# Kernel optimization log

Hardware: AMD Instinct MI355X
Metric: run time of the kernel (lower is better)

The kernel has to match this reference:

```python
import jax, jax.numpy as jnp
import numpy as np

B, T, D_IN, D_HID, D_OUT, N_CAT = 128, 64, 1024, 1024, 1536, 32


def setup_inputs() -> dict:
    key = jax.random.key(0)
    kx, kw1, kw2, kc = jax.random.split(key, 4)
    x = jax.random.normal(kx, (B, T, D_IN), dtype=jnp.float32)
    W1 = 0.02 * jax.random.normal(kw1, (N_CAT, D_IN, D_HID), dtype=jnp.float32)
    b1 = jnp.zeros((N_CAT, D_HID), dtype=jnp.float32)
    W2 = 0.02 * jax.random.normal(kw2, (N_CAT, D_HID, D_OUT), dtype=jnp.float32)
    b2 = jnp.zeros((N_CAT, D_OUT), dtype=jnp.float32)
    cat_ids = jax.random.randint(kc, (B,), 0, N_CAT)
    return {"x": x, "W1": W1, "b1": b1, "W2": W2, "b2": b2, "cat_ids": cat_ids}


def reference(x, W1, b1, W2, b2, cat_ids):
    # CategorySpecificLinear: gather per-sample expert weights, then batched matmul.
    # Layer 1: (B,T,D_in) @ (B,D_in,D_hid) + (B,1,D_hid)
    h = jnp.einsum('btd,bdh->bth', x, W1[cat_ids]) + b1[cat_ids][:, None, :]
    h = jax.nn.relu(h)
    # Layer 2: (B,T,D_hid) @ (B,D_hid,D_out) + (B,1,D_out)
    out = jnp.einsum('bth,bho->bto', h, W2[cat_ids]) + b2[cat_ids][:, None, :]
    return out
```

## Files before the change

kernel.cpp:

```cpp
#include <hip/hip_runtime.h>
#include <stdint.h>

#define NB    128
#define TT    64
#define KTOT  1024
#define DHID  1024
#define DOUT  1536
#define NCAT  32

#define BK    64
#define TN    128
#define PADR  72
#define NGMAX 64

typedef unsigned short u16;
typedef __attribute__((ext_vector_type(8))) short bf16x8;
typedef __attribute__((ext_vector_type(4))) float f32x4;
typedef __attribute__((ext_vector_type(4))) unsigned int uint4v;
typedef __attribute__((ext_vector_type(4))) float float4v;

__device__ __forceinline__ float bf2f(u16 u) {
    unsigned int x = ((unsigned int)u) << 16;
    return __builtin_bit_cast(float, x);
}
__device__ __forceinline__ unsigned int f2bf_u32(float f) {
    unsigned int x = __builtin_bit_cast(unsigned int, f);
    return (x + 0x7FFFu + ((x >> 16) & 1u)) >> 16;
}
__device__ __forceinline__ u16 f2bf(float f) { return (u16)f2bf_u32(f); }

__device__ int g_is_f32;

__global__ void detect_dtype(const unsigned int* __restrict__ xw) {
    const int lane = threadIdx.x;
    const unsigned int w = xw[lane * 64];
    const unsigned int e = (w >> 7) & 0xFF;
    const unsigned long long m = __ballot(e >= 120 && e <= 132);
    if (lane == 0) g_is_f32 = (__popcll(m) < 32) ? 1 : 0;
}

__device__ __forceinline__ void gload16(const void* g, void* l) {
    __builtin_amdgcn_global_load_lds(
        (const __attribute__((address_space(1))) void*)g,
        (__attribute__((address_space(3))) void*)l, 16, 0, 0);
}

__global__ void prep_x(const void* __restrict__ x, u16* __restrict__ xb) {
    const bool f32 = (g_is_f32 != 0);
    const size_t base = ((size_t)blockIdx.x * 256 + threadIdx.x) * 8;
    if (f32) {
        const float* s = (const float*)x + base;
        float4v f0 = *(const float4v*)s;
        float4v f1 = *(const float4v*)(s + 4);
        uint4v v;
        v.x = f2bf_u32(f0.x) | (f2bf_u32(f0.y) << 16);
        v.y = f2bf_u32(f0.z) | (f2bf_u32(f0.w) << 16);
        v.z = f2bf_u32(f1.x) | (f2bf_u32(f1.y) << 16);
        v.w = f2bf_u32(f1.z) | (f2bf_u32(f1.w) << 16);
        *(uint4v*)&xb[base] = v;
    } else {
        *(uint4v*)&xb[base] = *(const uint4v*)((const u16*)x + base);
    }
}

__global__ void build_groups(const int* __restrict__ cid,
                             int* __restrict__ gcat, int* __restrict__ gbat) {
    __shared__ int cl[NB];
    __shared__ int cnt[NCAT], start[NCAT], gbase[NCAT];
    __shared__ int sorted[NB];
    const int t = threadIdx.x;
    cl[t] = cid[t];
    if (t < NGMAX) gcat[t] = -1;
    gbat[t] = -1; gbat[NB + t] = -1;
    __syncthreads();
    if (t < NCAT) {
        int c = 0;
        for (int i = 0; i < NB; ++i) c += (cl[i] == t) ? 1 : 0;
        cnt[t] = c;
    }
    __syncthreads();
    if (t == 0) {
        int s = 0, g = 0;
        for (int c = 0; c < NCAT; ++c) {
            start[c] = s; s += cnt[c];
            gbase[c] = g; g += (cnt[c] + 3) >> 2;
        }
    }
    __syncthreads();
    {
        const int myc = cl[t];
        int r = 0;
        for (int i = 0; i < t; ++i) r += (cl[i] == myc) ? 1 : 0;
        sorted[start[myc] + r] = t;
    }
    __syncthreads();
    if (t < NCAT) {
        const int n = cnt[t], ng = (n + 3) >> 2;
        for (int j = 0; j < ng; ++j) {
            const int g = gbase[t] + j;
            gcat[g] = t;
            for (int k = 0; k < 4; ++k) {
                const int idx = j * 4 + k;
                gbat[g * 4 + k] = (idx < n) ? sorted[start[t] + idx] : -1;
            }
        }
    }
}

template<int NW, bool RELU, bool OUT_DYN>
__global__ __launch_bounds__(512, 4)
void gemm_grp(const u16* __restrict__ A,
              const void* __restrict__ Win,
              const void* __restrict__ BiasIn,
              void* __restrict__ Cout,
              const int* __restrict__ gcat,
              const int* __restrict__ gbat)
{
    constexpr int NT   = NW / TN;
    constexpr int NTIL = KTOT / 32;
    __shared__ __align__(16) u16 As[2][4 * TT * 32];
    __shared__ __align__(16) u16 Bs[2][TN * 32];

    const int nwg = NGMAX * NT;
    int bid = blockIdx.x;
    bid = (bid & 7) * (nwg >> 3) + (bid >> 3);
    const int g   = bid / NT;
    const int nt  = bid % NT;
    const int cat = gcat[g];
    if (cat < 0) return;

    const bool f32 = (g_is_f32 != 0);
    const int t    = threadIdx.x;
    const int wave = t >> 6;
    const int lane = t & 63;
    const int l16  = lane & 15;
    const int q    = lane >> 4;
    const int wm   = wave & 1;
    const int wn   = wave >> 1;

    const int bslot[4] = { gbat[g*4+0], gbat[g*4+1], gbat[g*4+2], gbat[g*4+3] };

    const int tt   = t & 255;
    const int arow = tt >> 2;
    const int asc  = (((tt & 3) ^ ((tt >> 2) & 3) ^ ((tt >> 4) & 3)) << 3);
    const int ah   = wave >> 2;
    const int sA0  = ah, sA1 = 2 + ah;
    const u16* aG0 = (bslot[sA0] >= 0)
        ? (A + (size_t)bslot[sA0] * (TT * KTOT) + (size_t)arow * KTOT + asc) : (const u16*)0;
    const u16* aG1 = (bslot[sA1] >= 0)
        ? (A + (size_t)bslot[sA1] * (TT * KTOT) + (size_t)arow * KTOT + asc) : (const u16*)0;

    const int bn  = t & 127;
    const int kc  = t >> 7;
    const int wch = ((kc ^ (bn & 3) ^ ((bn >> 2) & 3)) << 4);
    const size_t wOff = (size_t)cat * ((size_t)KTOT * NW) + (size_t)(kc * 8) * NW
                        + (size_t)nt * TN + bn;
    const float* w32 = (const float*)Win + wOff;
    const u16*   w16 = (const u16*)Win + wOff;

    const int CH = ((q ^ (l16 & 3) ^ ((l16 >> 2) & 3)) << 4);

    f32x4 acc[4][2][2];
#pragma unroll
    for (int bt = 0; bt < 4; ++bt)
#pragma unroll
        for (int im = 0; im < 2; ++im)
#pragma unroll
            for (int in = 0; in < 2; ++in)
                acc[bt][im][in] = (f32x4){0.f, 0.f, 0.f, 0.f};

    unsigned int wr[8];

    auto W_ISSUE = [&](int kk) {
        if (f32) {
            const float* ws = w32 + (size_t)kk * NW;
#pragma unroll
            for (int j = 0; j < 8; ++j)
                wr[j] = __builtin_bit_cast(unsigned int, ws[(size_t)j * NW]);
        } else {
            const u16* ws = w16 + (size_t)kk * NW;
#pragma unroll
            for (int j = 0; j < 8; ++j) wr[j] = ws[(size_t)j * NW];
        }
    };
    auto W_PACK = [&](int pb) {
        unsigned int p[4];
#pragma unroll
        for (int i = 0; i < 4; ++i) {
            unsigned int lo, hi;
            if (f32) {
                lo = f2bf_u32(__builtin_bit_cast(float, wr[2*i]));
                hi = f2bf_u32(__builtin_bit_cast(float, wr[2*i+1]));
            } else { lo = wr[2*i]; hi = wr[2*i+1]; }
            p[i] = lo | (hi << 16);
        }
        uint4v v; v.x = p[0]; v.y = p[1]; v.z = p[2]; v.w = p[3];
        *(uint4v*)((char*)&Bs[pb][0] + bn * 64 + wch) = v;
    };
    auto A_ISSUE = [&](int pb, int kk) {
        char* ab = (char*)&As[pb][0] + wave * 1024;
        if (aG0) gload16(aG0 + kk, ab);
        if (aG1) gload16(aG1 + kk, ab + 8192);
    };
    auto COMPUTE = [&](int pb) {
        const char* bsb = (const char*)&Bs[pb][0];
        const int nrow = wn * 32 + l16;
        bf16x8 bb0 = *(const bf16x8*)(bsb + nrow * 64 + CH);
        bf16x8 bb1 = *(const bf16x8*)(bsb + (nrow + 16) * 64 + CH);
        const char* asb = (const char*)&As[pb][0] + (wm * 32 + l16) * 64 + CH;
#pragma unroll
        for (int bt = 0; bt < 4; ++bt) {
            bf16x8 a0 = *(const bf16x8*)(asb + bt * 4096);
            bf16x8 a1 = *(const bf16x8*)(asb + bt * 4096 + 1024);
            acc[bt][0][0] = __builtin_amdgcn_mfma_f32_16x16x32_bf16(a0, bb0, acc[bt][0][0], 0, 0, 0);
            acc[bt][0][1] = __builtin_amdgcn_mfma_f32_16x16x32_bf16(a0, bb1, acc[bt][0][1], 0, 0, 0);
            acc[bt][1][0] = __builtin_amdgcn_mfma_f32_16x16x32_bf16(a1, bb0, acc[bt][1][0], 0, 0, 0);
            acc[bt][1][1] = __builtin_amdgcn_mfma_f32_16x16x32_bf16(a1, bb1, acc[bt][1][1], 0, 0, 0);
        }
    };

    W_ISSUE(0);
    A_ISSUE(0, 0);
    W_PACK(0);
    __syncthreads();

#pragma unroll 2
    for (int tl = 0; tl < NTIL; ++tl) {
        const int cur = tl & 1;
        if (tl + 1 < NTIL) {
            W_ISSUE((tl + 1) * 32);
            A_ISSUE(cur ^ 1, (tl + 1) * 32);
        }
        COMPUTE(cur);
        if (tl + 1 < NTIL) W_PACK(cur ^ 1);
        __syncthreads();
    }

    const float* bias32 = (const float*)BiasIn + (size_t)cat * NW + (size_t)nt * TN;
    const u16*   bias16 = (const u16*)BiasIn + (size_t)cat * NW + (size_t)nt * TN;
#pragma unroll
    for (int in = 0; in < 2; ++in) {
        const int ncol = wn * 32 + in * 16 + l16;
        const float bv = f32 ? bias32[ncol] : bf2f(bias16[ncol]);
#pragma unroll
        for (int bt = 0; bt < 4; ++bt) {
            const int b = bslot[bt];
            if (b < 0) continue;
            const size_t cOff = (size_t)b * (TT * NW) + (size_t)nt * TN + ncol;
#pragma unroll
            for (int im = 0; im < 2; ++im) {
#pragma unroll
                for (int r = 0; r < 4; ++r) {
                    const int m = wm * 32 + im * 16 + q * 4 + r;
                    float v = acc[bt][im][in][r] + bv;
                    if (RELU) v = fmaxf(v, 0.f);
                    if (OUT_DYN && f32) ((float*)Cout)[cOff + (size_t)m * NW] = v;
                    else                ((u16*)Cout)[cOff + (size_t)m * NW] = f2bf(v);
                }
            }
        }
    }
}

template<int NW, bool RELU, bool A_DYN, bool OUT_DYN>
__global__ __launch_bounds__(256, 4)
void gemm_cat(const void* __restrict__ Ain,
              const void* __restrict__ Win,
              const void* __restrict__ BiasIn,
              void* __restrict__ Cout,
              const int* __restrict__ cat_ids)
{
    constexpr int NT = NW / TN;
    __shared__ u16 As[TT * PADR];
    __shared__ u16 Bs[TN * PADR];

    const bool f32  = (g_is_f32 != 0);
    const bool aF32 = A_DYN && f32;
    const bool oF32 = OUT_DYN && f32;

    const int b   = blockIdx.x / NT;
    const int nt  = blockIdx.x % NT;
    const int cat = cat_ids[b];

    const int tid  = threadIdx.x;
    const int lane = tid & 63;
    const int l16  = lane & 15;
    const int q    = lane >> 4;
    const int wave = tid >> 6;
    const int wm   = wave & 1;
    const int wn   = wave >> 1;

    const size_t aOff = (size_t)b * (TT * KTOT);
    const u16*   Ab16 = (const u16*)Ain + aOff;
    const float* Ab32 = (const float*)Ain + aOff;
    const size_t wOff = (size_t)cat * ((size_t)KTOT * NW) + (size_t)nt * TN;
    const u16*   Wb16 = (const u16*)Win + wOff;
    const float* Wb32 = (const float*)Win + wOff;

    const int ar = tid >> 2;
    const int ac = (tid & 3) * 16;
    const int bn  = tid & 127;
    const int bk0 = tid >> 7;

    f32x4 acc[2][4];
#pragma unroll
    for (int im = 0; im < 2; ++im)
#pragma unroll
        for (int in = 0; in < 4; ++in)
            acc[im][in] = (f32x4){0.f, 0.f, 0.f, 0.f};

    for (int kk = 0; kk < KTOT; kk += BK) {
        if (!aF32) {
            const u16* src = Ab16 + ar * KTOT + kk + ac;
            uint4v v0 = *(const uint4v*)(src);
            uint4v v1 = *(const uint4v*)(src + 8);
            *(uint4v*)&As[ar * PADR + ac]     = v0;
            *(uint4v*)&As[ar * PADR + ac + 8] = v1;
        } else {
            const float* src = Ab32 + ar * KTOT + kk + ac;
            float4v f0 = *(const float4v*)(src);
            float4v f1 = *(const float4v*)(src + 4);
            float4v f2 = *(const float4v*)(src + 8);
            float4v f3 = *(const float4v*)(src + 12);
            uint4v v0, v1;
            v0.x = f2bf_u32(f0.x) | (f2bf_u32(f0.y) << 16);
            v0.y = f2bf_u32(f0.z) | (f2bf_u32(f0.w) << 16);
            v0.z = f2bf_u32(f1.x) | (f2bf_u32(f1.y) << 16);
            v0.w = f2bf_u32(f1.z) | (f2bf_u32(f1.w) << 16);
            v1.x = f2bf_u32(f2.x) | (f2bf_u32(f2.y) << 16);
            v1.y = f2bf_u32(f2.z) | (f2bf_u32(f2.w) << 16);
            v1.z = f2bf_u32(f3.x) | (f2bf_u32(f3.y) << 16);
            v1.w = f2bf_u32(f3.z) | (f2bf_u32(f3.w) << 16);
            *(uint4v*)&As[ar * PADR + ac]     = v0;
            *(uint4v*)&As[ar * PADR + ac + 8] = v1;
        }
#pragma unroll
        for (int i = 0; i < 4; ++i) {
            const int kc = bk0 + i * 2;
            unsigned int s[8];
            if (!f32) {
                const u16* src = Wb16 + (size_t)(kk + kc * 8) * NW + bn;
#pragma unroll
                for (int j = 0; j < 8; ++j) s[j] = src[(size_t)j * NW];
            } else {
                const float* src = Wb32 + (size_t)(kk + kc * 8) * NW + bn;
#pragma unroll
                for (int j = 0; j < 8; ++j) s[j] = f2bf_u32(src[(size_t)j * NW]);
            }
            uint4v v;
            v.x = s[0] | (s[1] << 16);
            v.y = s[2] | (s[3] << 16);
            v.z = s[4] | (s[5] << 16);
            v.w = s[6] | (s[7] << 16);
            *(uint4v*)&Bs[bn * PADR + kc * 8] = v;
        }
        __syncthreads();

#pragma unroll
        for (int s = 0; s < 2; ++s) {
            bf16x8 a[2], bb[4];
#pragma unroll
            for (int im = 0; im < 2; ++im)
                a[im] = *(const bf16x8*)&As[(wm * 32 + im * 16 + l16) * PADR + s * 32 + q * 8];
#pragma unroll
            for (int in = 0; in < 4; ++in)
                bb[in] = *(const bf16x8*)&Bs[(wn * 64 + in * 16 + l16) * PADR + s * 32 + q * 8];
#pragma unroll
            for (int im = 0; im < 2; ++im)
#pragma unroll
                for (int in = 0; in < 4; ++in)
                    acc[im][in] = __builtin_amdgcn_mfma_f32_16x16x32_bf16(
                        a[im], bb[in], acc[im][in], 0, 0, 0);
        }
        __syncthreads();
    }

    const u16*   bias16 = (const u16*)BiasIn + (size_t)cat * NW + nt * TN;
    const float* bias32 = (const float*)BiasIn + (size_t)cat * NW + nt * TN;
    const size_t cOff = (size_t)b * TT * NW + (size_t)nt * TN;
    u16*   C16 = (u16*)Cout + cOff;
    float* C32 = (float*)Cout + cOff;
#pragma unroll
    for (int in = 0; in < 4; ++in) {
        const int ncol = wn * 64 + in * 16 + l16;
        const float bv = f32 ? bias32[ncol] : bf2f(bias16[ncol]);
#pragma unroll
        for (int im = 0; im < 2; ++im) {
#pragma unroll
            for (int r = 0; r < 4; ++r) {
                const int m = wm * 32 + im * 16 + q * 4 + r;
                float v = acc[im][in][r] + bv;
                if (RELU) v = fmaxf(v, 0.f);
                if (oF32) C32[(size_t)m * NW + ncol] = v;
                else      C16[(size_t)m * NW + ncol] = f2bf(v);
            }
        }
    }
}

extern "C" void kernel_launch(void* const* d_in, const int* in_sizes, int n_in,
                              void* d_out, int out_size, void* d_ws, size_t ws_size,
                              hipStream_t stream) {
    const void* x   = d_in[0];
    const void* W1  = d_in[1];
    const void* b1  = d_in[2];
    const void* W2  = d_in[3];
    const void* b2  = d_in[4];
    const int*  cid = (const int*)d_in[5];

    const size_t XB_BYTES = (size_t)NB * TT * KTOT * 2;
    const size_t NEED = 2 * XB_BYTES + 4096;

    detect_dtype<<<1, 64, 0, stream>>>((const unsigned int*)x);

    if (ws_size >= NEED) {
        u16* xb   = (u16*)d_ws;
        u16* h    = (u16*)((char*)d_ws + XB_BYTES);
        int* gcat = (int*)((char*)d_ws + 2 * XB_BYTES);
        int* gbat = gcat + NGMAX;

        prep_x<<<4096, 256, 0, stream>>>(x, xb);
        build_groups<<<1, NB, 0, stream>>>(cid, gcat, gbat);
        gemm_grp<DHID, true,  false><<<NGMAX * (DHID / TN), 512, 0, stream>>>(
            xb, W1, b1, (void*)h, gcat, gbat);
        gemm_grp<DOUT, false, true ><<<NGMAX * (DOUT / TN), 512, 0, stream>>>(
            h, W2, b2, d_out, gcat, gbat);
    } else {
        u16* h = (u16*)d_ws;
        gemm_cat<DHID, true,  true,  false><<<NB * (DHID / TN), 256, 0, stream>>>(
            x, W1, b1, (void*)h, cid);
        gemm_cat<DOUT, false, false, true ><<<NB * (DOUT / TN), 256, 0, stream>>>(
            (const void*)h, W2, b2, d_out, cid);
    }
}
```

Baseline: 492.9 us.

## Fuse prep kernels, split barriers with manual waitcnt, remap block-to-group order

Merges the dtype detection, x conversion and group building into one kernel to cut launch count. In the grouped GEMM, the full __syncthreads is replaced with explicit s_waitcnt plus s_barrier and s_setprio around the MFMA compute, so loads stay in flight across the barrier. Empty batch slots now load a duplicate valid row instead of branching, and the block-to-group mapping is reordered. The risks are getting the hand-set vmcnt values wrong, which would race on LDS, and the extra redundant A loads for padded slots.

```diff
diff --git a/kernel.cpp b/kernel.cpp
--- a/kernel.cpp
+++ b/kernel.cpp
@@ -45,9 +45,22 @@
         (__attribute__((address_space(3))) void*)l, 16, 0, 0);
 }
 
-__global__ void prep_x(const void* __restrict__ x, u16* __restrict__ xb) {
-    const bool f32 = (g_is_f32 != 0);
-    const size_t base = ((size_t)blockIdx.x * 256 + threadIdx.x) * 8;
+__global__ void prep_all(const void* __restrict__ x, u16* __restrict__ xb,
+                         const int* __restrict__ cid,
+                         int* __restrict__ gcat, int* __restrict__ gbat) {
+    __shared__ int sh_f32;
+    const int t = threadIdx.x;
+    if (t < 64) {
+        const unsigned int w = ((const unsigned int*)x)[t * 64];
+        const unsigned int e = (w >> 7) & 0xFF;
+        const unsigned long long m = __ballot(e >= 120 && e <= 132);
+        if (t == 0) sh_f32 = (__popcll(m) < 32) ? 1 : 0;
+    }
+    __syncthreads();
+    const bool f32 = (sh_f32 != 0);
+    if (blockIdx.x == 0 && t == 0) g_is_f32 = f32 ? 1 : 0;
+
+    const size_t base = ((size_t)blockIdx.x * 256 + t) * 8;
     if (f32) {
         const float* s = (const float*)x + base;
         float4v f0 = *(const float4v*)s;
@@ -61,47 +74,45 @@
     } else {
         *(uint4v*)&xb[base] = *(const uint4v*)((const u16*)x + base);
     }
-}
-
-__global__ void build_groups(const int* __restrict__ cid,
-                             int* __restrict__ gcat, int* __restrict__ gbat) {
-    __shared__ int cl[NB];
-    __shared__ int cnt[NCAT], start[NCAT], gbase[NCAT];
-    __shared__ int sorted[NB];
-    const int t = threadIdx.x;
-    cl[t] = cid[t];
-    if (t < NGMAX) gcat[t] = -1;
-    gbat[t] = -1; gbat[NB + t] = -1;
-    __syncthreads();
-    if (t < NCAT) {
-        int c = 0;
-        for (int i = 0; i < NB; ++i) c += (cl[i] == t) ? 1 : 0;
-        cnt[t] = c;
-    }
-    __syncthreads();
-    if (t == 0) {
-        int s = 0, g = 0;
-        for (int c = 0; c < NCAT; ++c) {
-            start[c] = s; s += cnt[c];
-            gbase[c] = g; g += (cnt[c] + 3) >> 2;
-        }
-    }
-    __syncthreads();
-    {
-        const int myc = cl[t];
-        int r = 0;
-        for (int i = 0; i < t; ++i) r += (cl[i] == myc) ? 1 : 0;
-        sorted[start[myc] + r] = t;
-    }
-    __syncthreads();
-    if (t < NCAT) {
-        const int n = cnt[t], ng = (n + 3) >> 2;
-        for (int j = 0; j < ng; ++j) {
-            const int g = gbase[t] + j;
-            gcat[g] = t;
-            for (int k = 0; k < 4; ++k) {
-                const int idx = j * 4 + k;
-                gbat[g * 4 + k] = (idx < n) ? sorted[start[t] + idx] : -1;
+
+    if (blockIdx.x == 0) {
+        __shared__ int cl[NB];
+        __shared__ int cnt[NCAT], start[NCAT], gbase[NCAT];
+        __shared__ int sorted[NB];
+        if (t < NB) cl[t] = cid[t];
+        if (t < NGMAX) gcat[t] = -1;
+        gbat[t] = -1;
+        __syncthreads();
+        if (t < NCAT) {
+            int c = 0;
+            for (int i = 0; i < NB; ++i) c += (cl[i] == t) ? 1 : 0;
+            cnt[t] = c;
+        }
+        __syncthreads();
+        if (t == 0) {
+            int s = 0, g = 0;
+            for (int c = 0; c < NCAT; ++c) {
+                start[c] = s; s += cnt[c];
+                gbase[c] = g; g += (cnt[c] + 3) >> 2;
+            }
+        }
+        __syncthreads();
+        if (t < NB) {
+            const int myc = cl[t];
+            int r = 0;
+            for (int i = 0; i < t; ++i) r += (cl[i] == myc) ? 1 : 0;
+            sorted[start[myc] + r] = t;
+        }
+        __syncthreads();
+        if (t < NCAT) {
+            const int n = cnt[t], ng = (n + 3) >> 2;
+            for (int j = 0; j < ng; ++j) {
+                const int g = gbase[t] + j;
+                gcat[g] = t;
+                for (int k = 0; k < 4; ++k) {
+                    const int idx = j * 4 + k;
+                    gbat[g * 4 + k] = (idx < n) ? sorted[start[t] + idx] : -1;
+                }
             }
         }
     }
@@ -121,11 +132,10 @@
     __shared__ __align__(16) u16 As[2][4 * TT * 32];
     __shared__ __align__(16) u16 Bs[2][TN * 32];
 
-    const int nwg = NGMAX * NT;
-    int bid = blockIdx.x;
-    bid = (bid & 7) * (nwg >> 3) + (bid >> 3);
-    const int g   = bid / NT;
-    const int nt  = bid % NT;
+    const int bid = blockIdx.x;
+    const int qq  = bid >> 3;
+    const int nt  = qq % NT;
+    const int g   = (bid & 7) + 8 * (qq / NT);
     const int cat = gcat[g];
     if (cat < 0) return;
 
@@ -138,17 +148,18 @@
     const int wm   = wave & 1;
     const int wn   = wave >> 1;
 
-    const int bslot[4] = { gbat[g*4+0], gbat[g*4+1], gbat[g*4+2], gbat[g*4+3] };
+    int  bl[4]; bool lv[4];
+#pragma unroll
+    for (int k2 = 0; k2 < 4; ++k2) { int v = gbat[g * 4 + k2]; lv[k2] = (v >= 0); bl[k2] = v; }
+#pragma unroll
+    for (int k2 = 1; k2 < 4; ++k2) if (!lv[k2]) bl[k2] = bl[0];
 
     const int tt   = t & 255;
     const int arow = tt >> 2;
     const int asc  = (((tt & 3) ^ ((tt >> 2) & 3) ^ ((tt >> 4) & 3)) << 3);
-    const int ah   = wave >> 2;
-    const int sA0  = ah, sA1 = 2 + ah;
-    const u16* aG0 = (bslot[sA0] >= 0)
-        ? (A + (size_t)bslot[sA0] * (TT * KTOT) + (size_t)arow * KTOT + asc) : (const u16*)0;
-    const u16* aG1 = (bslot[sA1] >= 0)
-        ? (A + (size_t)bslot[sA1] * (TT * KTOT) + (size_t)arow * KTOT + asc) : (const u16*)0;
+    const int sA0  = wave >> 2, sA1 = 2 + (wave >> 2);
+    const u16* aG0 = A + (size_t)bl[sA0] * (TT * KTOT) + (size_t)arow * KTOT + asc;
+    const u16* aG1 = A + (size_t)bl[sA1] * (TT * KTOT) + (size_t)arow * KTOT + asc;
 
     const int bn  = t & 127;
     const int kc  = t >> 7;
@@ -199,8 +210,8 @@
     };
     auto A_ISSUE = [&](int pb, int kk) {
         char* ab = (char*)&As[pb][0] + wave * 1024;
-        if (aG0) gload16(aG0 + kk, ab);
-        if (aG1) gload16(aG1 + kk, ab + 8192);
+        gload16(aG0 + kk, ab);
+        gload16(aG1 + kk, ab + 8192);
     };
     auto COMPUTE = [&](int pb) {
         const char* bsb = (const char*)&Bs[pb][0];
@@ -221,8 +232,8 @@
 
     W_ISSUE(0);
     A_ISSUE(0, 0);
+    asm volatile("s_waitcnt vmcnt(2)" ::: "memory");
     W_PACK(0);
-    __syncthreads();
 
 #pragma unroll 2
     for (int tl = 0; tl < NTIL; ++tl) {
@@ -230,10 +241,19 @@
         if (tl + 1 < NTIL) {
             W_ISSUE((tl + 1) * 32);
             A_ISSUE(cur ^ 1, (tl + 1) * 32);
-        }
+            asm volatile("s_waitcnt vmcnt(10) lgkmcnt(0)" ::: "memory");
+        } else {
+            asm volatile("s_waitcnt vmcnt(0) lgkmcnt(0)" ::: "memory");
+        }
+        __builtin_amdgcn_s_barrier();
+        __builtin_amdgcn_s_setprio(1);
         COMPUTE(cur);
-        if (tl + 1 < NTIL) W_PACK(cur ^ 1);
-        __syncthreads();
+        __builtin_amdgcn_s_setprio(0);
+        if (tl + 1 < NTIL) {
+            asm volatile("s_waitcnt vmcnt(2)" ::: "memory");
+            W_PACK(cur ^ 1);
+            __builtin_amdgcn_s_barrier();
+        }
     }
 
     const float* bias32 = (const float*)BiasIn + (size_t)cat * NW + (size_t)nt * TN;
@@ -244,9 +264,8 @@
         const float bv = f32 ? bias32[ncol] : bf2f(bias16[ncol]);
 #pragma unroll
         for (int bt = 0; bt < 4; ++bt) {
-            const int b = bslot[bt];
-            if (b < 0) continue;
-            const size_t cOff = (size_t)b * (TT * NW) + (size_t)nt * TN + ncol;
+            if (!lv[bt]) continue;
+            const size_t cOff = (size_t)bl[bt] * (TT * NW) + (size_t)nt * TN + ncol;
 #pragma unroll
             for (int im = 0; im < 2; ++im) {
 #pragma unroll
@@ -411,22 +430,20 @@
     const size_t XB_BYTES = (size_t)NB * TT * KTOT * 2;
     const size_t NEED = 2 * XB_BYTES + 4096;
 
-    detect_dtype<<<1, 64, 0, stream>>>((const unsigned int*)x);
-
     if (ws_size >= NEED) {
         u16* xb   = (u16*)d_ws;
         u16* h    = (u16*)((char*)d_ws + XB_BYTES);
         int* gcat = (int*)((char*)d_ws + 2 * XB_BYTES);
         int* gbat = gcat + NGMAX;
 
-        prep_x<<<4096, 256, 0, stream>>>(x, xb);
-        build_groups<<<1, NB, 0, stream>>>(cid, gcat, gbat);
+        prep_all<<<4096, 256, 0, stream>>>(x, xb, cid, gcat, gbat);
         gemm_grp<DHID, true,  false><<<NGMAX * (DHID / TN), 512, 0, stream>>>(
             xb, W1, b1, (void*)h, gcat, gbat);
         gemm_grp<DOUT, false, true ><<<NGMAX * (DOUT / TN), 512, 0, stream>>>(
             h, W2, b2, d_out, gcat, gbat);
     } else {
         u16* h = (u16*)d_ws;
+        detect_dtype<<<1, 64, 0, stream>>>((const unsigned int*)x);
         gemm_cat<DHID, true,  true,  false><<<NB * (DHID / TN), 256, 0, stream>>>(
             x, W1, b1, (void*)h, cid);
         gemm_cat<DOUT, false, false, true ><<<NB * (DOUT / TN), 256, 0, stream>>>(
```

New measurement: 509.0 us. 1.03x slower.
